# Performance work log

Hardware: AMD Instinct MI355X
Metric: run time of the kernel (lower is better)

## Reference

```python
import jax, jax.numpy as jnp
import numpy as np

N = 50000
E = 1600000
F_IN = 503
F_H = 128
NEG_SLOPE = 0.2


def setup_inputs() -> dict:
    key = jax.random.key(0)
    ks = jax.random.split(key, 24)
    s = 0.05
    inp = {
        "x": jax.random.normal(ks[0], (N, F_IN), jnp.float32),
        "edge_index": jax.random.randint(ks[1], (2, E), 0, N, jnp.int64),
        "edge_attr": jax.random.uniform(ks[2], (E, 1), jnp.float32),
        "input_mask": jax.random.uniform(ks[3], (N, 1), jnp.float32),
        # GATConv layer 1 (in=503, out=128, heads=1, edge_dim=1)
        "W1": jax.random.normal(ks[4], (F_IN, F_H), jnp.float32) * s,
        "b1": jnp.zeros((F_H,), jnp.float32),
        "as1": jax.random.normal(ks[5], (F_H,), jnp.float32) * s,
        "ad1": jax.random.normal(ks[6], (F_H,), jnp.float32) * s,
        "We1": jax.random.normal(ks[7], (1, F_H), jnp.float32) * s,
        "ae1": jax.random.normal(ks[8], (F_H,), jnp.float32) * s,
        # GATConv layer 2 (in=128, out=128)
        "W2": jax.random.normal(ks[9], (F_H, F_H), jnp.float32) * s,
        "b2": jnp.zeros((F_H,), jnp.float32),
        "as2": jax.random.normal(ks[10], (F_H,), jnp.float32) * s,
        "ad2": jax.random.normal(ks[11], (F_H,), jnp.float32) * s,
        "We2": jax.random.normal(ks[12], (1, F_H), jnp.float32) * s,
        "ae2": jax.random.normal(ks[13], (F_H,), jnp.float32) * s,
        # edge/node heads
        "Wb": jax.random.normal(ks[14], (F_H, 1), jnp.float32) * s,
        "bb": jnp.zeros((1,), jnp.float32),
        "Ww": jax.random.normal(ks[15], (F_H, 1), jnp.float32) * s,
        "bw": jnp.zeros((1,), jnp.float32),
    }
    return inp


def _gat_conv(x, src, dst, ea, W, b, a_src_vec, a_dst_vec, We, a_edge_vec):
    """PyG GATConv, heads=1, add_self_loops=True, fill_value='mean'."""
    n = x.shape[0]
    loop = jnp.arange(n)
    # self-loop edge attrs = mean of incoming edge attrs (0 if none)
    deg = jax.ops.segment_sum(jnp.ones(dst.shape, ea.dtype), dst, num_segments=n)
    ea_loop = jax.ops.segment_sum(ea, dst, num_segments=n) / jnp.maximum(deg, 1.0)[:, None]
    s = jnp.concatenate([src, loop])
    d = jnp.concatenate([dst, loop])
    ea2 = jnp.concatenate([ea, ea_loop], axis=0)  # [E+N, 1]

    h = x @ W                              # [N, F_H]
    a_s = h @ a_src_vec                    # [N]
    a_d = h @ a_dst_vec                    # [N]
    a_e = (ea2 @ We) @ a_edge_vec          # [E+N]

    alpha = jax.nn.leaky_relu(a_s[s] + a_d[d] + a_e, NEG_SLOPE)
    # scatter-softmax over destination neighborhoods (every node has a self loop)
    m = jax.lax.stop_gradient(jax.ops.segment_max(alpha, d, num_segments=n))
    ex = jnp.exp(alpha - m[d])
    den = jax.ops.segment_sum(ex, d, num_segments=n)
    coef = ex / den[d]                     # [E+N]

    out = jax.ops.segment_sum(coef[:, None] * h[s], d, num_segments=n)
    return out + b


def reference(x, edge_index, edge_attr, input_mask,
              W1, b1, as1, ad1, We1, ae1,
              W2, b2, as2, ad2, We2, ae2,
              Wb, bb, Ww, bw):
    src, dst = edge_index[0], edge_index[1]
    h = jax.nn.relu(_gat_conv(x, src, dst, edge_attr, W1, b1, as1, ad1, We1, ae1))
    h = jax.nn.relu(_gat_conv(h, src, dst, edge_attr, W2, b2, as2, ad2, We2, ae2))
    b_out = (h @ Wb + bb) * input_mask          # [N, 1]
    # directed graph: is_directed() is True, so use all edges
    w = ((h[src] + h[dst]) * 0.5) @ Ww + bw     # [E, 1]
    return (w, b_out)
```

## Files before the change

kernel.cpp:

```cpp
#include <hip/hip_runtime.h>
#include <hip/hip_fp16.h>

#define FH 128
#define NEG_SLOPE 0.2f
#define GBM 64
#define GBK 64
#define HT 1024
#define TB 8
#define NWMAX 12512


typedef _Float16 f16x8 __attribute__((ext_vector_type(8)));
typedef float f32x4 __attribute__((ext_vector_type(4)));

__global__ __launch_bounds__(HT) void hist_kernel(const int* __restrict__ ei,
                                                  unsigned short* __restrict__ hist,
                                                  int E, int N) {
  __shared__ unsigned int lh[NWMAX];
  const int b = blockIdx.x, tid = threadIdx.x;
  const int nw = (N + 3) >> 2;
  for (int j = tid; j < nw; j += HT) lh[j] = 0u;
  __syncthreads();
  const int i0 = b * (HT * TB) + tid * TB;
  if (i0 + TB <= E) {
    int4 da = *(const int4*)&ei[E + i0];
    int4 db = *(const int4*)&ei[E + i0 + 4];
    int dv[8] = {da.x, da.y, da.z, da.w, db.x, db.y, db.z, db.w};
    #pragma unroll
    for (int k = 0; k < 8; k++)
      atomicAdd(&lh[dv[k] >> 2], 1u << ((dv[k] & 3) * 8));
  } else {
    for (int i = i0; i < E; i++) {
      int d = ei[E + i];
      atomicAdd(&lh[d >> 2], 1u << ((d & 3) * 8));
    }
  }
  __syncthreads();
  unsigned short* hb = hist + (size_t)b * N;
  for (int j = tid; j < nw; j += HT) {
    unsigned v = lh[j];
    int bin = j * 4;
    if (bin + 3 < N) {
      ushort4 o;
      o.x = v & 255u; o.y = (v >> 8) & 255u; o.z = (v >> 16) & 255u; o.w = v >> 24;
      *(ushort4*)&hb[bin] = o;
    } else {
      for (int k = 0; k < 4 && bin + k < N; k++) hb[bin + k] = (v >> (k * 8)) & 255u;
    }
  }
}

__global__ void colscan_kernel(unsigned short* __restrict__ hist,
                               int* __restrict__ cnt, int N, int NBr) {
  int bin = blockIdx.x * 256 + threadIdx.x;
  if (bin >= N) return;
  int s = 0, b = 0;
  for (; b + 8 <= NBr; b += 8) {
    int t[8];
    #pragma unroll
    for (int k = 0; k < 8; k++) t[k] = hist[(size_t)(b + k) * N + bin];
    #pragma unroll
    for (int k = 0; k < 8; k++) {
      hist[(size_t)(b + k) * N + bin] = (unsigned short)s;
      s += t[k];
    }
  }
  for (; b < NBr; b++) {
    int t = hist[(size_t)b * N + bin];
    hist[(size_t)b * N + bin] = (unsigned short)s;
    s += t;
  }
  cnt[bin] = s;
}

__global__ void scan_blocksum(const int* __restrict__ deg, int* __restrict__ bsum, int n) {
  __shared__ int sm[256];
  int i = blockIdx.x * 256 + threadIdx.x;
  sm[threadIdx.x] = (i < n) ? deg[i] : 0;
  __syncthreads();
  for (int off = 128; off > 0; off >>= 1) {
    if (threadIdx.x < off) sm[threadIdx.x] += sm[threadIdx.x + off];
    __syncthreads();
  }
  if (threadIdx.x == 0) bsum[blockIdx.x] = sm[0];
}

__global__ void scan_bsum(int* __restrict__ bsum, int nb, int* __restrict__ rowptr, int N) {
  __shared__ int sm[1024];
  int t = threadIdx.x;
  int v = (t < nb) ? bsum[t] : 0;
  sm[t] = v;
  __syncthreads();
  for (int off = 1; off < 1024; off <<= 1) {
    int u = (t >= off) ? sm[t - off] : 0;
    __syncthreads();
    sm[t] += u;
    __syncthreads();
  }
  if (t < nb) bsum[t] = sm[t] - v;
  if (t == 1023) rowptr[N] = sm[1023];
}

__global__ void scan_final(const int* __restrict__ deg, const int* __restrict__ bsum,
                           int* __restrict__ rowptr, int n) {
  __shared__ int sm[256];
  int i = blockIdx.x * 256 + threadIdx.x;
  int v = (i < n) ? deg[i] : 0;
  sm[threadIdx.x] = v;
  __syncthreads();
  for (int off = 1; off < 256; off <<= 1) {
    int u = (threadIdx.x >= off) ? sm[threadIdx.x - off] : 0;
    __syncthreads();
    sm[threadIdx.x] += u;
    __syncthreads();
  }
  if (i < n) rowptr[i] = bsum[blockIdx.x] + sm[threadIdx.x] - v;
}

__global__ __launch_bounds__(HT) void place_kernel(const int* __restrict__ ei,
                                                   const float* __restrict__ ea,
                                                   const int* __restrict__ rowptr,
                                                   const unsigned short* __restrict__ off,
                                                   unsigned int* __restrict__ pack,
                                                   int E, int N) {
  __shared__ unsigned int lc[NWMAX];
  const int b = blockIdx.x, tid = threadIdx.x;
  const int nw = (N + 3) >> 2;
  for (int j = tid; j < nw; j += HT) lc[j] = 0u;
  __syncthreads();
  const unsigned short* __restrict__ ob = off + (size_t)b * N;
  const int i0 = b * (HT * TB) + tid * TB;
  if (i0 + TB <= E) {
    int4 sa = *(const int4*)&ei[i0];
    int4 sb = *(const int4*)&ei[i0 + 4];
    int4 da = *(const int4*)&ei[E + i0];
    int4 db = *(const int4*)&ei[E + i0 + 4];
    float4 aa = *(const float4*)&ea[i0];
    float4 ab = *(const float4*)&ea[i0 + 4];
    int sv[8] = {sa.x, sa.y, sa.z, sa.w, sb.x, sb.y, sb.z, sb.w};
    int dv[8] = {da.x, da.y, da.z, da.w, db.x, db.y, db.z, db.w};
    float av[8] = {aa.x, aa.y, aa.z, aa.w, ab.x, ab.y, ab.z, ab.w};
    unsigned rr[8];
    #pragma unroll
    for (int k = 0; k < 8; k++)
      rr[k] = atomicAdd(&lc[dv[k] >> 2], 1u << ((dv[k] & 3) * 8));
    int pos[8];
    #pragma unroll
    for (int k = 0; k < 8; k++)
      pos[k] = rowptr[dv[k]] + (int)ob[dv[k]] + (int)((rr[k] >> ((dv[k] & 3) * 8)) & 255u);
    #pragma unroll
    for (int k = 0; k < 8; k++)
      pack[pos[k]] = ((unsigned)sv[k] << 16) | __half_as_ushort(__float2half(av[k]));
  } else {
    for (int i = i0; i < E; i++) {
      int d = ei[E + i];
      unsigned r = atomicAdd(&lc[d >> 2], 1u << ((d & 3) * 8));
      int local = (r >> ((d & 3) * 8)) & 255;
      int pos = rowptr[d] + (int)ob[d] + local;
      pack[pos] = ((unsigned)ei[i] << 16) | __half_as_ushort(__float2half(ea[i]));
    }
  }
}

__global__ void cvec_kernel(const float* __restrict__ We1, const float* __restrict__ ae1,
                            const float* __restrict__ We2, const float* __restrict__ ae2,
                            float* __restrict__ cv) {
  int l = threadIdx.x;
  float s1 = We1[l] * ae1[l] + We1[l + 64] * ae1[l + 64];
  float s2 = We2[l] * ae2[l] + We2[l + 64] * ae2[l + 64];
  for (int off = 32; off; off >>= 1) { s1 += __shfl_down(s1, off); s2 += __shfl_down(s2, off); }
  if (l == 0) { cv[0] = s1; cv[1] = s2; }
}

__global__ void wcvt_kernel(const float* __restrict__ W, __half* __restrict__ Wt,
                            int K, int Kpad, int perm) {
  int idx = blockIdx.x * 256 + threadIdx.x;
  if (idx >= 128 * Kpad) return;
  int n = idx / Kpad, p = idx - n * Kpad;
  int k = perm ? ((p & 7) * 16 + (p >> 3)) : p;
  Wt[idx] = (k < K) ? __float2half(W[(size_t)k * 128 + n]) : __float2half(0.f);
}

__global__ __launch_bounds__(256) void xpack_kernel(const float* __restrict__ X,
                                                    __half* __restrict__ A16,
                                                    int M, int K, int Kpad) {
  __shared__ _Float16 T[64 * 16 * 8];
  const int mg = blockIdx.x, tid = threadIdx.x;
  const int nq = Kpad >> 3;
  const int r = tid >> 4, qs = tid & 15;
  const float* __restrict__ Xr = X + (size_t)(mg * 16 + r) * K;
  for (int q = qs; q < nq; q += 16) {
    f16x8 v;
    int kb = q * 8;
    #pragma unroll
    for (int j = 0; j < 8; j++)
      v[j] = (kb + j < K) ? (_Float16)Xr[kb + j] : (_Float16)0.f;
    *(f16x8*)&T[(q * 16 + r) * 8] = v;
  }
  __syncthreads();
  const int total = nq * 128;
  _Float16* dst = (_Float16*)A16 + (size_t)mg * total;
  for (int o = tid * 8; o < total; o += 256 * 8)
    *(f16x8*)&dst[o] = *(const f16x8*)&T[o];
}

__global__ __launch_bounds__(256, 4) void mfma_gemm_kernel(
    const __half* __restrict__ A16_, const __half* __restrict__ Wt_,
    const float* __restrict__ avs, const float* __restrict__ avd,
    __half* __restrict__ H16, float* __restrict__ a_s, float* __restrict__ a_d,
    int M, int Kpad) {
  __shared__ _Float16 Bl[2 * 8 * 64 * 8];
  const _Float16* __restrict__ A16 = (const _Float16*)A16_;
  const _Float16* __restrict__ Wt  = (const _Float16*)Wt_;
  const int tid  = threadIdx.x;
  const int lane = tid & 63;
  const int w    = tid >> 6;
  const int m0   = blockIdx.x * GBM;
  const int nq   = Kpad >> 3;

  f32x4 acc[8];
  #pragma unroll
  for (int i = 0; i < 8; i++) acc[i] = (f32x4){0.f, 0.f, 0.f, 0.f};

  const int mgc = min(m0 / 16 + w, M / 16 - 1);
  const _Float16* __restrict__ Abase =
      A16 + (size_t)mgc * nq * 128 + (lane >> 4) * 128 + (lane & 15) * 8;

  const int sg = tid & 7, snb = tid >> 3;

  for (int k0 = 0; k0 < Kpad; k0 += GBK) {
    #pragma unroll
    for (int i = 0; i < 4; i++) {
      int n = snb + 32 * i;
      f16x8 v = *(const f16x8*)(Wt + (size_t)n * Kpad + k0 + sg * 8);
      int kt = sg >> 2, nt = n >> 4;
      int fl = (n & 15) + (sg & 3) * 16;
      *(f16x8*)&Bl[((kt * 8 + nt) * 64 + fl) * 8] = v;
    }
    __syncthreads();
    #pragma unroll
    for (int kt = 0; kt < 2; kt++) {
      f16x8 af = *(const f16x8*)(Abase + (size_t)k0 * 16 + kt * 512);
      #pragma unroll
      for (int nt = 0; nt < 8; nt++) {
        f16x8 bf = *(const f16x8*)&Bl[((kt * 8 + nt) * 64 + lane) * 8];
        acc[nt] = __builtin_amdgcn_mfma_f32_16x16x32_f16(af, bf, acc[nt], 0, 0, 0);
      }
    }
    __syncthreads();
  }

  const int rbase = m0 + w * 16 + (lane >> 4) * 4;
  const int col   = lane & 15;
  float as_v[8], ad_v[8];
  #pragma unroll
  for (int nt = 0; nt < 8; nt++) {
    as_v[nt] = avs[nt * 16 + col];
    ad_v[nt] = avd[nt * 16 + col];
  }
  #pragma unroll
  for (int r = 0; r < 4; r++) {
    int gm = rbase + r;
    float ps = 0.f, pd = 0.f;
    #pragma unroll
    for (int nt = 0; nt < 8; nt++) {
      ps += acc[nt][r] * as_v[nt];
      pd += acc[nt][r] * ad_v[nt];
    }
    #pragma unroll
    for (int msk = 1; msk < 16; msk <<= 1) {
      ps += __shfl_xor(ps, msk);
      pd += __shfl_xor(pd, msk);
    }
    if (gm < M) {
      __half2 h0 = __floats2half2_rn(acc[0][r], acc[1][r]);
      __half2 h1 = __floats2half2_rn(acc[2][r], acc[3][r]);
      __half2 h2 = __floats2half2_rn(acc[4][r], acc[5][r]);
      __half2 h3 = __floats2half2_rn(acc[6][r], acc[7][r]);
      uint4 u;
      u.x = *(unsigned*)&h0; u.y = *(unsigned*)&h1;
      u.z = *(unsigned*)&h2; u.w = *(unsigned*)&h3;
      *(uint4*)&H16[(size_t)gm * FH + col * 8] = u;
      if (col == 0) { a_s[gm] = ps; a_d[gm] = pd; }
    }
  }
}

template<int OUTP>
__global__ __launch_bounds__(256) void agg_kernel(
    const __half* __restrict__ H16, const int* __restrict__ rowptr,
    const unsigned int* __restrict__ pack,
    const float* __restrict__ a_s, const float* __restrict__ a_d,
    const float* __restrict__ cv, int cidx,
    const float* __restrict__ bias,
    float* __restrict__ HoutF, __half* __restrict__ HoutP, int N) {
  const int node = (blockIdx.x * 256 + threadIdx.x) >> 6;
  const int lane = threadIdx.x & 63;
  const int slot = lane >> 4, sl = lane & 15;
  if (node >= N) return;
  const _Float16* __restrict__ Hh = (const _Float16*)H16;
  const float c   = cv[cidx];
  const float adn = a_d[node];
  const int beg = rowptr[node], end = rowptr[node + 1];

  float acc[8] = {0.f, 0.f, 0.f, 0.f, 0.f, 0.f, 0.f, 0.f};
  float accB[8] = {0.f, 0.f, 0.f, 0.f, 0.f, 0.f, 0.f, 0.f};
  float den = 0.f, ea_tot = 0.f, denB = 0.f, eaB = 0.f;

  int p = beg + slot;
  for (; p + 4 < end; p += 8) {
    unsigned w0 = pack[p], w1 = pack[p + 4];
    int s0 = w0 >> 16, s1 = w1 >> 16;
    float e0 = __half2float(__ushort_as_half((unsigned short)(w0 & 0xffff)));
    float e1 = __half2float(__ushort_as_half((unsigned short)(w1 & 0xffff)));
    float as0 = a_s[s0], as1 = a_s[s1];
    f16x8 h0 = *(const f16x8*)(Hh + (size_t)s0 * FH + sl * 8);
    f16x8 h1 = *(const f16x8*)(Hh + (size_t)s1 * FH + sl * 8);
    float al0 = as0 + adn + c * e0;
    float al1 = as1 + adn + c * e1;
    al0 = fmaxf(al0, NEG_SLOPE * al0);
    al1 = fmaxf(al1, NEG_SLOPE * al1);
    float ex0 = __expf(al0), ex1 = __expf(al1);
    ea_tot += e0; eaB += e1;
    den += ex0; denB += ex1;
    #pragma unroll
    for (int j = 0; j < 8; j++) {
      acc[j]  += ex0 * (float)h0[j];
      accB[j] += ex1 * (float)h1[j];
    }
  }
  for (; p < end; p += 4) {
    unsigned w0 = pack[p];
    int s0 = w0 >> 16;
    float e0 = __half2float(__ushort_as_half((unsigned short)(w0 & 0xffff)));
    float al = a_s[s0] + adn + c * e0;
    al = fmaxf(al, NEG_SLOPE * al);
    float ex = __expf(al);
    f16x8 h = *(const f16x8*)(Hh + (size_t)s0 * FH + sl * 8);
    ea_tot += e0;
    den += ex;
    #pragma unroll
    for (int j = 0; j < 8; j++) acc[j] += ex * (float)h[j];
  }
  den += denB; ea_tot += eaB;
  #pragma unroll
  for (int j = 0; j < 8; j++) acc[j] += accB[j];
  ea_tot += __shfl_xor(ea_tot, 16); ea_tot += __shfl_xor(ea_tot, 32);
  den    += __shfl_xor(den,    16); den    += __shfl_xor(den,    32);
  #pragma unroll
  for (int j = 0; j < 8; j++) {
    acc[j] += __shfl_xor(acc[j], 16);
    acc[j] += __shfl_xor(acc[j], 32);
  }
  {
    int dg = end - beg;
    float eal = ea_tot / fmaxf((float)dg, 1.f);
    float al = a_s[node] + adn + c * eal;
    al = fmaxf(al, NEG_SLOPE * al);
    float ex = __expf(al);
    f16x8 h = *(const f16x8*)(Hh + (size_t)node * FH + sl * 8);
    den += ex;
    #pragma unroll
    for (int j = 0; j < 8; j++) acc[j] += ex * (float)h[j];
  }
  if (slot == 0) {
    float inv = 1.f / den;
    float v[8];
    #pragma unroll
    for (int j = 0; j < 8; j++)
      v[j] = fmaxf(acc[j] * inv + bias[j * 16 + sl], 0.f);
    if (OUTP) {
      f16x8 o;
      #pragma unroll
      for (int j = 0; j < 8; j++) o[j] = (_Float16)v[j];
      int mg = node >> 4, r = node & 15;
      *(f16x8*)((_Float16*)HoutP + (((size_t)mg * 16 + sl) * 16 + r) * 8) = o;
    } else {
      float4 o0 = make_float4(v[0], v[1], v[2], v[3]);
      float4 o1 = make_float4(v[4], v[5], v[6], v[7]);
      *(float4*)&HoutF[(size_t)node * FH + sl * 8]     = o0;
      *(float4*)&HoutF[(size_t)node * FH + sl * 8 + 4] = o1;
    }
  }
}

__global__ void node_head_kernel(const float* __restrict__ H, const float* __restrict__ Wb,
                                 const float* __restrict__ bb, const float* __restrict__ Ww,
                                 const float* __restrict__ mask,
                                 float* __restrict__ bout, float* __restrict__ p, int N) {
  int gid = blockIdx.x * 256 + threadIdx.x;
  int node = gid >> 6, lane = threadIdx.x & 63;
  if (node >= N) return;
  int p0 = lane * 2, p1 = p0 + 1;
  int f0 = ((p0 & 7) << 4) + (p0 >> 3);
  int f1 = ((p1 & 7) << 4) + (p1 >> 3);
  float2 h = *(const float2*)&H[(size_t)node * FH + p0];
  float sb = h.x * Wb[f0] + h.y * Wb[f1];
  float sw = h.x * Ww[f0] + h.y * Ww[f1];
  for (int off = 32; off; off >>= 1) { sb += __shfl_down(sb, off); sw += __shfl_down(sw, off); }
  if (lane == 0) {
    bout[node] = (sb + bb[0]) * mask[node];
    p[node]    = sw;
  }
}

__global__ void edge_head_kernel(const int* __restrict__ ei, const float* __restrict__ p,
                                 const float* __restrict__ bw, float* __restrict__ w, int E) {
  int base = (blockIdx.x * 256 + threadIdx.x) * 4;
  if (base >= E) return;
  float b = bw[0];
  if (base + 4 <= E) {
    int4 s = *(const int4*)&ei[base];
    int4 d = *(const int4*)&ei[E + base];
    float4 o;
    o.x = 0.5f * (p[s.x] + p[d.x]) + b;
    o.y = 0.5f * (p[s.y] + p[d.y]) + b;
    o.z = 0.5f * (p[s.z] + p[d.z]) + b;
    o.w = 0.5f * (p[s.w] + p[d.w]) + b;
    *(float4*)&w[base] = o;
  } else {
    for (int e = base; e < E; e++)
      w[e] = 0.5f * (p[ei[e]] + p[ei[E + e]]) + b;
  }
}

extern "C" void kernel_launch(void* const* d_in, const int* in_sizes, int n_in,
                              void* d_out, int out_size, void* d_ws, size_t ws_size,
                              hipStream_t stream) {
  (void)n_in; (void)out_size; (void)ws_size;
  const float* x    = (const float*)d_in[0];
  const int*   ei   = (const int*)  d_in[1];
  const float* ea   = (const float*)d_in[2];
  const float* mask = (const float*)d_in[3];
  const float* W1   = (const float*)d_in[4];
  const float* b1   = (const float*)d_in[5];
  const float* as1  = (const float*)d_in[6];
  const float* ad1  = (const float*)d_in[7];
  const float* We1  = (const float*)d_in[8];
  const float* ae1  = (const float*)d_in[9];
  const float* W2   = (const float*)d_in[10];
  const float* b2   = (const float*)d_in[11];
  const float* as2  = (const float*)d_in[12];
  const float* ad2  = (const float*)d_in[13];
  const float* We2  = (const float*)d_in[14];
  const float* ae2  = (const float*)d_in[15];
  const float* Wb   = (const float*)d_in[16];
  const float* bb   = (const float*)d_in[17];
  const float* Ww   = (const float*)d_in[18];
  const float* bw   = (const float*)d_in[19];

  const int N  = in_sizes[3];
  const int E  = in_sizes[1] / 2;
  const int K1 = in_sizes[0] / N;
  const int K1p = (K1 + GBK - 1) & ~(GBK - 1);
  const int NBr = (E + HT * TB - 1) / (HT * TB);
  const int NT  = N / 16;

  char* ws = (char*)d_ws;
  size_t off0 = 0;
  auto alloc = [&](size_t bytes) -> char* {
    char* q = ws + off0;
    off0 = (off0 + bytes + 255) & ~(size_t)255;
    return q;
  };
  int*   cnt    = (int*)  alloc((size_t)N * 4);
  int*   rowptr = (int*)  alloc((size_t)(N + 1) * 4);
  int*   bsum   = (int*)  alloc(1024 * 4);
  size_t uszA = (size_t)NBr * N * 2;
  size_t uszB = (size_t)NT * (K1p / 8) * 256;
  char*  uni  = alloc(uszA > uszB ? uszA : uszB);
  unsigned short* hist = (unsigned short*)uni;
  __half* XA16 = (__half*)uni;
  __half* HB16 = (__half*)uni;
  unsigned int* pack = (unsigned int*)alloc((size_t)E * 4);
  float* a_s    = (float*)alloc((size_t)N * 4);
  float* a_d    = (float*)alloc((size_t)N * 4);
  __half* H16   = (__half*)alloc((size_t)N * FH * 2);
  float* HB     = (float*)alloc((size_t)N * FH * 4);
  float* pbuf   = (float*)alloc((size_t)N * 4);
  float* cv     = (float*)alloc(8);
  __half* W1t   = (__half*)alloc((size_t)FH * K1p * 2);
  __half* W2t   = (__half*)alloc((size_t)FH * FH * 2);

  float* w_out = (float*)d_out;
  float* b_out = (float*)d_out + E;

  const int nb  = (N + 255) / 256;
  const int gb  = (N + GBM - 1) / GBM;
  const int wbk = ((size_t)N * 64 + 255) / 256;
  const int ab  = (N + 3) / 4;
  const int eb4 = (E + 1023) / 1024;

  hist_kernel   <<<NBr, HT, 0, stream>>>(ei, hist, E, N);
  colscan_kernel<<<nb, 256, 0, stream>>>(hist, cnt, N, NBr);
  scan_blocksum <<<nb, 256, 0, stream>>>(cnt, bsum, N);
  scan_bsum     <<<1, 1024, 0, stream>>>(bsum, nb, rowptr, N);
  scan_final    <<<nb, 256, 0, stream>>>(cnt, bsum, rowptr, N);
  place_kernel  <<<NBr, HT, 0, stream>>>(ei, ea, rowptr, hist, pack, E, N);
  cvec_kernel   <<<1, 64, 0, stream>>>(We1, ae1, We2, ae2, cv);
  wcvt_kernel   <<<(128 * K1p + 255) / 256, 256, 0, stream>>>(W1, W1t, K1, K1p, 0);
  wcvt_kernel   <<<(128 * FH + 255) / 256, 256, 0, stream>>>(W2, W2t, FH, FH, 1);
  xpack_kernel  <<<NT, 256, 0, stream>>>(x, XA16, N, K1, K1p);

  mfma_gemm_kernel<<<gb, 256, 0, stream>>>(XA16, W1t, as1, ad1, H16, a_s, a_d, N, K1p);
  agg_kernel<1><<<ab, 256, 0, stream>>>(H16, rowptr, pack, a_s, a_d, cv, 0, b1,
                                        nullptr, HB16, N);
  mfma_gemm_kernel<<<gb, 256, 0, stream>>>(HB16, W2t, as2, ad2, H16, a_s, a_d, N, FH);
  agg_kernel<0><<<ab, 256, 0, stream>>>(H16, rowptr, pack, a_s, a_d, cv, 1, b2,
                                        HB, nullptr, N);
  node_head_kernel<<<wbk, 256, 0, stream>>>(HB, Wb, bb, Ww, mask, b_out, pbuf, N);
  edge_head_kernel<<<eb4, 256, 0, stream>>>(ei, pbuf, bw, w_out, E);
}
```

Baseline: 315.0 us.

## Fuse X fp16 packing into GEMM and node heads into layer-2 aggregation

```diff
diff --git a/kernel.cpp b/kernel.cpp
--- a/kernel.cpp
+++ b/kernel.cpp
@@ -8,6 +8,7 @@
 #define HT 1024
 #define TB 8
 #define NWMAX 12512
+#define ALS 68
 
 
 typedef _Float16 f16x8 __attribute__((ext_vector_type(8)));
@@ -181,50 +182,32 @@
   Wt[idx] = (k < K) ? __float2half(W[(size_t)k * 128 + n]) : __float2half(0.f);
 }
 
-__global__ __launch_bounds__(256) void xpack_kernel(const float* __restrict__ X,
-                                                    __half* __restrict__ A16,
-                                                    int M, int K, int Kpad) {
-  __shared__ _Float16 T[64 * 16 * 8];
-  const int mg = blockIdx.x, tid = threadIdx.x;
-  const int nq = Kpad >> 3;
-  const int r = tid >> 4, qs = tid & 15;
-  const float* __restrict__ Xr = X + (size_t)(mg * 16 + r) * K;
-  for (int q = qs; q < nq; q += 16) {
-    f16x8 v;
-    int kb = q * 8;
-    #pragma unroll
-    for (int j = 0; j < 8; j++)
-      v[j] = (kb + j < K) ? (_Float16)Xr[kb + j] : (_Float16)0.f;
-    *(f16x8*)&T[(q * 16 + r) * 8] = v;
-  }
-  __syncthreads();
-  const int total = nq * 128;
-  _Float16* dst = (_Float16*)A16 + (size_t)mg * total;
-  for (int o = tid * 8; o < total; o += 256 * 8)
-    *(f16x8*)&dst[o] = *(const f16x8*)&T[o];
-}
-
+template<int STAGEA>
 __global__ __launch_bounds__(256, 4) void mfma_gemm_kernel(
-    const __half* __restrict__ A16_, const __half* __restrict__ Wt_,
+    const float* __restrict__ Xf, const __half* __restrict__ A16_,
+    const __half* __restrict__ Wt_,
     const float* __restrict__ avs, const float* __restrict__ avd,
     __half* __restrict__ H16, float* __restrict__ a_s, float* __restrict__ a_d,
-    int M, int Kpad) {
+    int M, int K, int Kpad) {
   __shared__ _Float16 Bl[2 * 8 * 64 * 8];
-  const _Float16* __restrict__ A16 = (const _Float16*)A16_;
-  const _Float16* __restrict__ Wt  = (const _Float16*)Wt_;
+  __shared__ float Af[STAGEA ? 64 * ALS : 1];
+  const _Float16* __restrict__ Wt = (const _Float16*)Wt_;
   const int tid  = threadIdx.x;
   const int lane = tid & 63;
   const int w    = tid >> 6;
   const int m0   = blockIdx.x * GBM;
-  const int nq   = Kpad >> 3;
 
   f32x4 acc[8];
   #pragma unroll
   for (int i = 0; i < 8; i++) acc[i] = (f32x4){0.f, 0.f, 0.f, 0.f};
 
-  const int mgc = min(m0 / 16 + w, M / 16 - 1);
-  const _Float16* __restrict__ Abase =
-      A16 + (size_t)mgc * nq * 128 + (lane >> 4) * 128 + (lane & 15) * 8;
+  const _Float16* Abase = nullptr;
+  if constexpr (!STAGEA) {
+    const int nq = Kpad >> 3;
+    const int mgc = min(m0 / 16 + w, M / 16 - 1);
+    Abase = (const _Float16*)A16_ + (size_t)mgc * nq * 128 +
+            (lane >> 4) * 128 + (lane & 15) * 8;
+  }
 
   const int sg = tid & 7, snb = tid >> 3;
 
@@ -237,10 +220,28 @@
       int fl = (n & 15) + (sg & 3) * 16;
       *(f16x8*)&Bl[((kt * 8 + nt) * 64 + fl) * 8] = v;
     }
+    if constexpr (STAGEA) {
+      #pragma unroll
+      for (int i = 0; i < 16; i++) {
+        int e = i * 256 + tid;
+        int row = e >> 6, col = e & 63;
+        int gm = m0 + row, gk = k0 + col;
+        float v = 0.f;
+        if (gm < M && gk < K) v = Xf[(size_t)gm * K + gk];
+        Af[row * ALS + col] = v;
+      }
+    }
     __syncthreads();
     #pragma unroll
     for (int kt = 0; kt < 2; kt++) {
-      f16x8 af = *(const f16x8*)(Abase + (size_t)k0 * 16 + kt * 512);
+      f16x8 af;
+      if constexpr (STAGEA) {
+        const float* ap = &Af[(w * 16 + (lane & 15)) * ALS + kt * 32 + (lane >> 4) * 8];
+        #pragma unroll
+        for (int j = 0; j < 8; j++) af[j] = (_Float16)ap[j];
+      } else {
+        af = *(const f16x8*)(Abase + (size_t)k0 * 16 + kt * 512);
+      }
       #pragma unroll
       for (int nt = 0; nt < 8; nt++) {
         f16x8 bf = *(const f16x8*)&Bl[((kt * 8 + nt) * 64 + lane) * 8];
@@ -293,7 +294,10 @@
     const float* __restrict__ a_s, const float* __restrict__ a_d,
     const float* __restrict__ cv, int cidx,
     const float* __restrict__ bias,
-    float* __restrict__ HoutF, __half* __restrict__ HoutP, int N) {
+    __half* __restrict__ HoutP,
+    const float* __restrict__ Wb, const float* __restrict__ bb,
+    const float* __restrict__ Ww, const float* __restrict__ mask,
+    float* __restrict__ bout, float* __restrict__ pbuf, int N) {
   const int node = (blockIdx.x * 256 + threadIdx.x) >> 6;
   const int lane = threadIdx.x & 63;
   const int slot = lane >> 4, sl = lane & 15;
@@ -376,31 +380,23 @@
       int mg = node >> 4, r = node & 15;
       *(f16x8*)((_Float16*)HoutP + (((size_t)mg * 16 + sl) * 16 + r) * 8) = o;
     } else {
-      float4 o0 = make_float4(v[0], v[1], v[2], v[3]);
-      float4 o1 = make_float4(v[4], v[5], v[6], v[7]);
-      *(float4*)&HoutF[(size_t)node * FH + sl * 8]     = o0;
-      *(float4*)&HoutF[(size_t)node * FH + sl * 8 + 4] = o1;
-    }
-  }
-}
-
-__global__ void node_head_kernel(const float* __restrict__ H, const float* __restrict__ Wb,
-                                 const float* __restrict__ bb, const float* __restrict__ Ww,
-                                 const float* __restrict__ mask,
-                                 float* __restrict__ bout, float* __restrict__ p, int N) {
-  int gid = blockIdx.x * 256 + threadIdx.x;
-  int node = gid >> 6, lane = threadIdx.x & 63;
-  if (node >= N) return;
-  int p0 = lane * 2, p1 = p0 + 1;
-  int f0 = ((p0 & 7) << 4) + (p0 >> 3);
-  int f1 = ((p1 & 7) << 4) + (p1 >> 3);
-  float2 h = *(const float2*)&H[(size_t)node * FH + p0];
-  float sb = h.x * Wb[f0] + h.y * Wb[f1];
-  float sw = h.x * Ww[f0] + h.y * Ww[f1];
-  for (int off = 32; off; off >>= 1) { sb += __shfl_down(sb, off); sw += __shfl_down(sw, off); }
-  if (lane == 0) {
-    bout[node] = (sb + bb[0]) * mask[node];
-    p[node]    = sw;
+      float sb = 0.f, sw = 0.f;
+      #pragma unroll
+      for (int j = 0; j < 8; j++) {
+        int f = j * 16 + sl;
+        sb += v[j] * Wb[f];
+        sw += v[j] * Ww[f];
+      }
+      #pragma unroll
+      for (int m = 1; m < 16; m <<= 1) {
+        sb += __shfl_xor(sb, m);
+        sw += __shfl_xor(sw, m);
+      }
+      if (sl == 0) {
+        bout[node] = (sb + bb[0]) * mask[node];
+        pbuf[node] = sw;
+      }
+    }
   }
 }
 
@@ -454,7 +450,6 @@
   const int K1 = in_sizes[0] / N;
   const int K1p = (K1 + GBK - 1) & ~(GBK - 1);
   const int NBr = (E + HT * TB - 1) / (HT * TB);
-  const int NT  = N / 16;
 
   char* ws = (char*)d_ws;
   size_t off0 = 0;
@@ -467,16 +462,14 @@
   int*   rowptr = (int*)  alloc((size_t)(N + 1) * 4);
   int*   bsum   = (int*)  alloc(1024 * 4);
   size_t uszA = (size_t)NBr * N * 2;
-  size_t uszB = (size_t)NT * (K1p / 8) * 256;
+  size_t uszB = (size_t)N * FH * 2;
   char*  uni  = alloc(uszA > uszB ? uszA : uszB);
   unsigned short* hist = (unsigned short*)uni;
-  __half* XA16 = (__half*)uni;
   __half* HB16 = (__half*)uni;
   unsigned int* pack = (unsigned int*)alloc((size_t)E * 4);
   float* a_s    = (float*)alloc((size_t)N * 4);
   float* a_d    = (float*)alloc((size_t)N * 4);
   __half* H16   = (__half*)alloc((size_t)N * FH * 2);
-  float* HB     = (float*)alloc((size_t)N * FH * 4);
   float* pbuf   = (float*)alloc((size_t)N * 4);
   float* cv     = (float*)alloc(8);
   __half* W1t   = (__half*)alloc((size_t)FH * K1p * 2);
@@ -487,7 +480,6 @@
 
   const int nb  = (N + 255) / 256;
   const int gb  = (N + GBM - 1) / GBM;
-  const int wbk = ((size_t)N * 64 + 255) / 256;
   const int ab  = (N + 3) / 4;
   const int eb4 = (E + 1023) / 1024;
 
@@ -500,14 +492,15 @@
   cvec_kernel   <<<1, 64, 0, stream>>>(We1, ae1, We2, ae2, cv);
   wcvt_kernel   <<<(128 * K1p + 255) / 256, 256, 0, stream>>>(W1, W1t, K1, K1p, 0);
   wcvt_kernel   <<<(128 * FH + 255) / 256, 256, 0, stream>>>(W2, W2t, FH, FH, 1);
-  xpack_kernel  <<<NT, 256, 0, stream>>>(x, XA16, N, K1, K1p);
-
-  mfma_gemm_kernel<<<gb, 256, 0, stream>>>(XA16, W1t, as1, ad1, H16, a_s, a_d, N, K1p);
+
+  mfma_gemm_kernel<1><<<gb, 256, 0, stream>>>(x, nullptr, W1t, as1, ad1,
+                                              H16, a_s, a_d, N, K1, K1p);
   agg_kernel<1><<<ab, 256, 0, stream>>>(H16, rowptr, pack, a_s, a_d, cv, 0, b1,
-                                        nullptr, HB16, N);
-  mfma_gemm_kernel<<<gb, 256, 0, stream>>>(HB16, W2t, as2, ad2, H16, a_s, a_d, N, FH);
+                                        HB16, nullptr, nullptr, nullptr, nullptr,
+                                        nullptr, nullptr, N);
+  mfma_gemm_kernel<0><<<gb, 256, 0, stream>>>(nullptr, HB16, W2t, as2, ad2,
+                                              H16, a_s, a_d, N, FH, FH);
   agg_kernel<0><<<ab, 256, 0, stream>>>(H16, rowptr, pack, a_s, a_d, cv, 1, b2,
-                                        HB, nullptr, N);
-  node_head_kernel<<<wbk, 256, 0, stream>>>(HB, Wb, bb, Ww, mask, b_out, pbuf, N);
+                                        nullptr, Wb, bb, Ww, mask, b_out, pbuf, N);
   edge_head_kernel<<<eb4, 256, 0, stream>>>(ei, pbuf, bw, w_out, E);
 }
```

New measurement: 270.5 us. 1.16x faster.
